# Kernel optimization log

Hardware: AMD Instinct MI355X
Metric: run time of the kernel (lower is better)

Reference implementation:

```python
import jax, jax.numpy as jnp
import numpy as np

D_MODEL = 1024
N_HEADS = 16
D_HEAD = D_MODEL // N_HEADS


def setup_inputs() -> dict:
    key = jax.random.key(0)
    ks = jax.random.split(key, 9)
    B, S = 2, 2048
    s = 0.02
    return {
        "x": jax.random.normal(ks[0], (B, S, D_MODEL), dtype=jnp.float32),
        "Wq": jax.random.normal(ks[1], (D_MODEL, D_MODEL), dtype=jnp.float32) * s,
        "bq": jnp.zeros((D_MODEL,), dtype=jnp.float32),
        "Wk": jax.random.normal(ks[2], (D_MODEL, D_MODEL), dtype=jnp.float32) * s,
        "bk": jnp.zeros((D_MODEL,), dtype=jnp.float32),
        "Wv": jax.random.normal(ks[3], (D_MODEL, D_MODEL), dtype=jnp.float32) * s,
        "bv": jnp.zeros((D_MODEL,), dtype=jnp.float32),
        "Wo": jax.random.normal(ks[4], (D_MODEL, D_MODEL), dtype=jnp.float32) * s,
        "bo": jnp.zeros((D_MODEL,), dtype=jnp.float32),
    }


def reference(x, Wq, bq, Wk, bk, Wv, bv, Wo, bo):
    B, S, _ = x.shape
    # projections -> [B, H, S, Dh]
    def split_heads(t):
        return t.reshape(B, S, N_HEADS, D_HEAD).transpose(0, 2, 1, 3)
    Q = split_heads(x @ Wq + bq)
    K = split_heads(x @ Wk + bk)
    V = split_heads(x @ Wv + bv)
    scores = jnp.einsum('bhqd,bhkd->bhqk', Q, K)  # [B,H,S,S]
    mask = jnp.tril(jnp.ones((S, S), dtype=bool))
    # NB: original masks BEFORE scaling (mask fill -1e9 then /sqrt(d_head))
    scores = jnp.where(mask[None, None], scores, jnp.float32(-1e9))
    scores = scores / jnp.sqrt(jnp.float32(D_HEAD))
    attn = jax.nn.softmax(scores, axis=-1)
    ctx = jnp.einsum('bhqk,bhkd->bhqd', attn, V)
    ctx = ctx.transpose(0, 2, 1, 3).reshape(B, S, D_MODEL)
    return ctx @ Wo + bo
```

## Files before the change

kernel.cpp:

```cpp
#include <hip/hip_runtime.h>

typedef __bf16 bf16;
typedef __bf16 bf16x8 __attribute__((ext_vector_type(8)));
typedef __bf16 bf16x4 __attribute__((ext_vector_type(4)));
typedef float  f32x4  __attribute__((ext_vector_type(4)));

#define D_MODEL 1024
#define S_LEN   2048
#define NHEAD   16
#define DHEAD   64
#define BATCH   2
#define MROWS   (BATCH * S_LEN)

#define QSCALE 0.18033688011112042f

__device__ __forceinline__ void gld_lds16(const void* g, void* lds_base) {
    __builtin_amdgcn_global_load_lds(
        (const __attribute__((address_space(1))) void*)g,
        (__attribute__((address_space(3))) void*)lds_base, 16, 0, 0);
}

__global__ void prep_kernel(const float* __restrict__ x,
                            const float* __restrict__ W0, const float* __restrict__ W1,
                            const float* __restrict__ W2, const float* __restrict__ W3,
                            bf16* __restrict__ xb, bf16* __restrict__ Wt) {
    int tx = threadIdx.x, ty = threadIdx.y;
    if (blockIdx.z == 4) {
        int tid = ty * 32 + tx;
        size_t base = ((size_t)blockIdx.y * 32 + blockIdx.x) * 4096;
#pragma unroll
        for (int j = 0; j < 4; j++) {
            size_t i = base + (size_t)(j * 256 + tid) * 4;
            f32x4 v = *(const f32x4*)(x + i);
            bf16x4 o;
            o[0] = (bf16)v[0]; o[1] = (bf16)v[1]; o[2] = (bf16)v[2]; o[3] = (bf16)v[3];
            *(bf16x4*)(xb + i) = o;
        }
        return;
    }
    __shared__ float tile[32][33];
    const float* W = (blockIdx.z == 0) ? W0 : (blockIdx.z == 1) ? W1
                   : (blockIdx.z == 2) ? W2 : W3;
    int n0 = blockIdx.x * 32, k0 = blockIdx.y * 32;
#pragma unroll
    for (int j = 0; j < 4; j++)
        tile[ty + 8 * j][tx] = W[(size_t)(k0 + ty + 8 * j) * D_MODEL + n0 + tx];
    __syncthreads();
    bf16* out = Wt + (size_t)blockIdx.z * D_MODEL * D_MODEL;
#pragma unroll
    for (int j = 0; j < 4; j++)
        out[(size_t)(n0 + ty + 8 * j) * D_MODEL + k0 + tx] = (bf16)tile[tx][ty + 8 * j];
}

template <int MODE>
__global__ __launch_bounds__(256, 2) void gemm_kernel(
    const bf16* __restrict__ A, const bf16* __restrict__ Bt,
    const float* __restrict__ b0, const float* __restrict__ b1, const float* __restrict__ b2,
    bf16* __restrict__ Qo, bf16* __restrict__ Ko, bf16* __restrict__ Vto,
    float* __restrict__ Co) {
    __shared__ bf16 sA[128 * 32];
    __shared__ bf16 sB[128 * 32];
    const int t = threadIdx.x;
    const int wave = t >> 6, lane = t & 63;
    const int wm = wave >> 1, wn = wave & 1;
    const int quad = lane >> 4, m16 = lane & 15;
    const int row0 = blockIdx.y * 128, col0 = blockIdx.x * 128;
    const int K = D_MODEL;

    f32x4 acc[4][4];
#pragma unroll
    for (int i = 0; i < 4; i++)
#pragma unroll
        for (int j = 0; j < 4; j++) acc[i][j] = (f32x4){0.f, 0.f, 0.f, 0.f};

    for (int kk = 0; kk < K; kk += 32) {
#pragma unroll
        for (int i = 0; i < 2; i++) {
            int cb = i * 256 + wave * 64;
            int c  = cb + lane;
            int r  = c >> 2, kg = c & 3;
            gld_lds16(A  + (size_t)(row0 + r) * K + kk + kg * 8, (char*)sA + cb * 16);
            gld_lds16(Bt + (size_t)(col0 + r) * K + kk + kg * 8, (char*)sB + cb * 16);
        }
        __syncthreads();
        bf16x8 af[4], bfr[4];
#pragma unroll
        for (int mi = 0; mi < 4; mi++)
            af[mi] = *(const bf16x8*)&sA[(wm * 64 + mi * 16 + m16) * 32 + quad * 8];
#pragma unroll
        for (int ni = 0; ni < 4; ni++)
            bfr[ni] = *(const bf16x8*)&sB[(wn * 64 + ni * 16 + m16) * 32 + quad * 8];
#pragma unroll
        for (int mi = 0; mi < 4; mi++)
#pragma unroll
            for (int ni = 0; ni < 4; ni++)
                acc[mi][ni] = __builtin_amdgcn_mfma_f32_16x16x32_bf16(
                    af[mi], bfr[ni], acc[mi][ni], 0, 0, 0);
        __syncthreads();
    }

    if (MODE == 1) {
#pragma unroll
        for (int mi = 0; mi < 4; mi++) {
            int r0 = row0 + wm * 64 + mi * 16 + quad * 4;
#pragma unroll
            for (int ni = 0; ni < 4; ni++) {
                int col = col0 + wn * 64 + ni * 16 + m16;
                float bias = b0[col];
#pragma unroll
                for (int r = 0; r < 4; r++)
                    Co[(size_t)(r0 + r) * D_MODEL + col] = acc[mi][ni][r] + bias;
            }
        }
    } else {
        int sel = col0 >> 10;
        const float* bias_arr = (sel == 0) ? b0 : (sel == 1) ? b1 : b2;
#pragma unroll
        for (int mi = 0; mi < 4; mi++) {
            int s0g = row0 + wm * 64 + mi * 16 + quad * 4;
            int b = s0g >> 11, ss0 = s0g & 2047;
#pragma unroll
            for (int ni = 0; ni < 4; ni++) {
                int col = col0 + wn * 64 + ni * 16 + m16;
                int cn = col & 1023;
                int h = cn >> 6, d = cn & 63;
                float bias = bias_arr[cn];
                if (sel < 2) {
                    bf16* dst = (sel == 0) ? Qo : Ko;
                    float scl = (sel == 0) ? QSCALE : 1.0f;
                    size_t base = (((size_t)b * NHEAD + h) * S_LEN);
#pragma unroll
                    for (int r = 0; r < 4; r++)
                        dst[(base + ss0 + r) * DHEAD + d] = (bf16)((acc[mi][ni][r] + bias) * scl);
                } else {
                    bf16x4 pk;
#pragma unroll
                    for (int r = 0; r < 4; r++) pk[r] = (bf16)(acc[mi][ni][r] + bias);
                    *(bf16x4*)(Vto + (((size_t)b * NHEAD + h) * DHEAD + d) * S_LEN + ss0) = pk;
                }
            }
        }
    }
}

__global__ __launch_bounds__(256, 3) void attn_kernel(
    const bf16* __restrict__ Q, const bf16* __restrict__ K,
    const bf16* __restrict__ Vt, bf16* __restrict__ ctx) {
    __shared__ bf16 Kt_s[2][64 * 64];
    __shared__ bf16 Vt_s[2][64 * 64];
    __shared__ bf16 P_s[4][2][16 * 72];

    const int t = threadIdx.x, wave = t >> 6, lane = t & 63;
    const int quad = lane >> 4, m16 = lane & 15;
    const int bh = blockIdx.y;
    const int tile = gridDim.x - 1 - blockIdx.x;
    const int q0 = tile * 128;
    const size_t qkbase = (size_t)bh * S_LEN * DHEAD;
    const int nt = 2 * tile + 2;

    bf16x8 aq[2][2];
#pragma unroll
    for (int g = 0; g < 2; g++)
#pragma unroll
        for (int kst = 0; kst < 2; kst++)
            aq[g][kst] = *(const bf16x8*)(Q + qkbase
                + (size_t)(q0 + wave * 32 + g * 16 + m16) * DHEAD + kst * 32 + quad * 8);

    f32x4 o[2][4];
#pragma unroll
    for (int g = 0; g < 2; g++)
#pragma unroll
        for (int di = 0; di < 4; di++) o[g][di] = (f32x4){0.f, 0.f, 0.f, 0.f};
    float l_acc[2] = {0.f, 0.f};

#pragma unroll
    for (int i = 0; i < 2; i++) {
        int cb = i * 256 + wave * 64;
        int c  = cb + lane;
        int pos = c >> 3, g = c & 7;
        int gk = g ^ (pos & 7);
        gld_lds16(K  + qkbase + (size_t)pos * DHEAD + gk * 8, (char*)&Kt_s[0][0] + cb * 16);
        gld_lds16(Vt + qkbase + (size_t)pos * S_LEN + gk * 8, (char*)&Vt_s[0][0] + cb * 16);
    }
    __syncthreads();

    for (int it = 0; it < nt; ++it) {
        const int cur = it & 1;
        const int kt0 = it * 64;
        if (it + 1 < nt) {
            const int ktn = kt0 + 64;
#pragma unroll
            for (int i = 0; i < 2; i++) {
                int cb = i * 256 + wave * 64;
                int c  = cb + lane;
                int pos = c >> 3, g = c & 7;
                int gk = g ^ (pos & 7);
                gld_lds16(K  + qkbase + (size_t)(ktn + pos) * DHEAD + gk * 8,
                          (char*)&Kt_s[cur ^ 1][0] + cb * 16);
                gld_lds16(Vt + qkbase + (size_t)pos * S_LEN + ktn + gk * 8,
                          (char*)&Vt_s[cur ^ 1][0] + cb * 16);
            }
        }

        f32x4 sc[2][4];
#pragma unroll
        for (int g = 0; g < 2; g++)
#pragma unroll
            for (int ni = 0; ni < 4; ni++) sc[g][ni] = (f32x4){0.f, 0.f, 0.f, 0.f};
#pragma unroll
        for (int ni = 0; ni < 4; ni++) {
            int pos = ni * 16 + m16;
#pragma unroll
            for (int kst = 0; kst < 2; kst++) {
                int gg = (kst * 4 + quad) ^ (pos & 7);
                bf16x8 kf = *(const bf16x8*)&Kt_s[cur][pos * 64 + gg * 8];
#pragma unroll
                for (int g = 0; g < 2; g++)
                    sc[g][ni] = __builtin_amdgcn_mfma_f32_16x16x32_bf16(
                        kf, aq[g][kst], sc[g][ni], 0, 0, 0);
            }
        }
#pragma unroll
        for (int g = 0; g < 2; g++) {
            int rowbase = q0 + wave * 32 + g * 16;
            if (kt0 + 63 > rowbase) {
                int qg = rowbase + m16;
#pragma unroll
                for (int ni = 0; ni < 4; ni++)
#pragma unroll
                    for (int r = 0; r < 4; r++) {
                        int kp = kt0 + ni * 16 + quad * 4 + r;
                        if (kp > qg) sc[g][ni][r] = -1e9f;
                    }
            }
        }
#pragma unroll
        for (int g = 0; g < 2; g++) {
            bf16* Pw = &P_s[wave][g][0];
            float ls = 0.f;
#pragma unroll
            for (int ni = 0; ni < 4; ni++) {
                bf16x4 pk;
#pragma unroll
                for (int r = 0; r < 4; r++) {
                    float p = __builtin_amdgcn_exp2f(sc[g][ni][r]);
                    ls += p;
                    pk[r] = (bf16)p;
                }
                *(bf16x4*)&Pw[m16 * 72 + ni * 16 + quad * 4] = pk;
            }
            l_acc[g] += ls;
        }

#pragma unroll
        for (int kst = 0; kst < 2; kst++) {
            bf16x8 ap[2];
#pragma unroll
            for (int g = 0; g < 2; g++)
                ap[g] = *(const bf16x8*)&P_s[wave][g][m16 * 72 + kst * 32 + quad * 8];
#pragma unroll
            for (int di = 0; di < 4; di++) {
                int d = di * 16 + m16;
                int gg = (kst * 4 + quad) ^ (d & 7);
                bf16x8 vf = *(const bf16x8*)&Vt_s[cur][d * 64 + gg * 8];
#pragma unroll
                for (int g = 0; g < 2; g++)
                    o[g][di] = __builtin_amdgcn_mfma_f32_16x16x32_bf16(
                        vf, ap[g], o[g][di], 0, 0, 0);
            }
        }
        __syncthreads();
    }

    int b = bh >> 4, h = bh & 15;
#pragma unroll
    for (int g = 0; g < 2; g++) {
        float l = l_acc[g];
        l += __shfl_xor(l, 16);
        l += __shfl_xor(l, 32);
        float rl = 1.0f / l;
        int s = q0 + wave * 32 + g * 16 + m16;
#pragma unroll
        for (int di = 0; di < 4; di++) {
            bf16x4 pk;
#pragma unroll
            for (int r = 0; r < 4; r++) pk[r] = (bf16)(o[g][di][r] * rl);
            *(bf16x4*)(ctx + ((size_t)b * S_LEN + s) * D_MODEL
                       + h * DHEAD + di * 16 + quad * 4) = pk;
        }
    }
}

extern "C" void kernel_launch(void* const* d_in, const int* in_sizes, int n_in,
                              void* d_out, int out_size, void* d_ws, size_t ws_size,
                              hipStream_t stream) {
    const float* x  = (const float*)d_in[0];
    const float* Wq = (const float*)d_in[1];
    const float* bq = (const float*)d_in[2];
    const float* Wk = (const float*)d_in[3];
    const float* bk = (const float*)d_in[4];
    const float* Wv = (const float*)d_in[5];
    const float* bv = (const float*)d_in[6];
    const float* Wo = (const float*)d_in[7];
    const float* bo = (const float*)d_in[8];
    float* out = (float*)d_out;

    char* ws = (char*)d_ws;
    const size_t MB = 1u << 20;
    bf16* xb  = (bf16*)(ws + 0);
    bf16* Wt  = (bf16*)(ws + 8  * MB);
    bf16* Qb  = (bf16*)(ws + 16 * MB);
    bf16* Kb  = (bf16*)(ws + 24 * MB);
    bf16* Vtb = (bf16*)(ws + 32 * MB);
    bf16* ctx = (bf16*)(ws + 0);

    prep_kernel<<<dim3(32, 32, 5), dim3(32, 8), 0, stream>>>(x, Wq, Wk, Wv, Wo, xb, Wt);
    gemm_kernel<0><<<dim3(24, 32), 256, 0, stream>>>(xb, Wt, bq, bk, bv,
                                                     Qb, Kb, Vtb, nullptr);
    attn_kernel<<<dim3(16, 32), 256, 0, stream>>>(Qb, Kb, Vtb, ctx);
    gemm_kernel<1><<<dim3(8, 32), 256, 0, stream>>>(ctx, Wt + 3 * 1024 * 1024,
                                                    bo, nullptr, nullptr,
                                                    nullptr, nullptr, nullptr, out);
}
```

Before: 201.1 us.

## Pair causal query tiles for balanced work and triple-buffer K/V loads

Each block now processes two 64-row query tiles, p and 31-p, so every block does the same amount of causal work instead of a variable amount per 128-row tile. K/V staging moves to a three-deep LDS ring with one barrier per step, using explicit vmcnt waits in place of the end-of-loop __syncthreads. The mask is applied only on each tile's diagonal block. In exchange LDS use grows, the launch bound drops to 2 blocks per CU, and the inline-asm waitcnt depends on the load count per stage.

Measured after the change: 191.0 us. 1.05x faster.

```diff
diff --git a/kernel.cpp b/kernel.cpp
--- a/kernel.cpp
+++ b/kernel.cpp
@@ -143,148 +143,151 @@
     }
 }
 
-__global__ __launch_bounds__(256, 3) void attn_kernel(
+__global__ __launch_bounds__(256, 2) void attn_kernel(
     const bf16* __restrict__ Q, const bf16* __restrict__ K,
     const bf16* __restrict__ Vt, bf16* __restrict__ ctx) {
-    __shared__ bf16 Kt_s[2][64 * 64];
-    __shared__ bf16 Vt_s[2][64 * 64];
+    __shared__ bf16 Kt_s[3][64 * 64];
+    __shared__ bf16 Vt_s[3][64 * 64];
     __shared__ bf16 P_s[4][2][16 * 72];
 
     const int t = threadIdx.x, wave = t >> 6, lane = t & 63;
     const int quad = lane >> 4, m16 = lane & 15;
-    const int bh = blockIdx.y;
-    const int tile = gridDim.x - 1 - blockIdx.x;
-    const int q0 = tile * 128;
-    const size_t qkbase = (size_t)bh * S_LEN * DHEAD;
-    const int nt = 2 * tile + 2;
+    const int bh = blockIdx.y, p = blockIdx.x;
+    const int tT[2] = {p, 31 - p};
+    const int nt = 32 - p;
+    const size_t base = (size_t)bh * S_LEN * DHEAD;
 
     bf16x8 aq[2][2];
 #pragma unroll
-    for (int g = 0; g < 2; g++)
+    for (int it = 0; it < 2; it++)
 #pragma unroll
         for (int kst = 0; kst < 2; kst++)
-            aq[g][kst] = *(const bf16x8*)(Q + qkbase
-                + (size_t)(q0 + wave * 32 + g * 16 + m16) * DHEAD + kst * 32 + quad * 8);
+            aq[it][kst] = *(const bf16x8*)(Q + base
+                + (size_t)(tT[it] * 64 + wave * 16 + m16) * DHEAD + kst * 32 + quad * 8);
 
     f32x4 o[2][4];
 #pragma unroll
-    for (int g = 0; g < 2; g++)
-#pragma unroll
-        for (int di = 0; di < 4; di++) o[g][di] = (f32x4){0.f, 0.f, 0.f, 0.f};
+    for (int it = 0; it < 2; it++)
+#pragma unroll
+        for (int di = 0; di < 4; di++) o[it][di] = (f32x4){0.f, 0.f, 0.f, 0.f};
     float l_acc[2] = {0.f, 0.f};
 
-#pragma unroll
-    for (int i = 0; i < 2; i++) {
-        int cb = i * 256 + wave * 64;
-        int c  = cb + lane;
-        int pos = c >> 3, g = c & 7;
-        int gk = g ^ (pos & 7);
-        gld_lds16(K  + qkbase + (size_t)pos * DHEAD + gk * 8, (char*)&Kt_s[0][0] + cb * 16);
-        gld_lds16(Vt + qkbase + (size_t)pos * S_LEN + gk * 8, (char*)&Vt_s[0][0] + cb * 16);
-    }
-    __syncthreads();
-
-    for (int it = 0; it < nt; ++it) {
-        const int cur = it & 1;
-        const int kt0 = it * 64;
-        if (it + 1 < nt) {
-            const int ktn = kt0 + 64;
-#pragma unroll
-            for (int i = 0; i < 2; i++) {
-                int cb = i * 256 + wave * 64;
-                int c  = cb + lane;
-                int pos = c >> 3, g = c & 7;
-                int gk = g ^ (pos & 7);
-                gld_lds16(K  + qkbase + (size_t)(ktn + pos) * DHEAD + gk * 8,
-                          (char*)&Kt_s[cur ^ 1][0] + cb * 16);
-                gld_lds16(Vt + qkbase + (size_t)pos * S_LEN + ktn + gk * 8,
-                          (char*)&Vt_s[cur ^ 1][0] + cb * 16);
-            }
-        }
-
-        f32x4 sc[2][4];
-#pragma unroll
-        for (int g = 0; g < 2; g++)
-#pragma unroll
-            for (int ni = 0; ni < 4; ni++) sc[g][ni] = (f32x4){0.f, 0.f, 0.f, 0.f};
-#pragma unroll
-        for (int ni = 0; ni < 4; ni++) {
-            int pos = ni * 16 + m16;
+    auto stage = [&](int j, int buf) {
+#pragma unroll
+        for (int i = 0; i < 2; i++) {
+            int cb = i * 256 + wave * 64;
+            int c  = cb + lane;
+            int pos = c >> 3, g = c & 7;
+            int gk = g ^ (pos & 7);
+            gld_lds16(K  + base + (size_t)(j * 64 + pos) * DHEAD + gk * 8,
+                      (char*)&Kt_s[buf][0] + cb * 16);
+            gld_lds16(Vt + base + (size_t)pos * S_LEN + j * 64 + gk * 8,
+                      (char*)&Vt_s[buf][0] + cb * 16);
+        }
+    };
+
+    stage(0, 0);
+    if (nt > 1) stage(1, 1);
+
+    for (int j = 0; j < nt; ++j) {
+        if (j + 1 < nt) asm volatile("s_waitcnt vmcnt(4)\n\ts_barrier" ::: "memory");
+        else            asm volatile("s_waitcnt vmcnt(0)\n\ts_barrier" ::: "memory");
+        if (j + 2 < nt) stage(j + 2, (j + 2) % 3);
+
+        const int cur = j % 3;
+        const bool aAct = (j <= tT[0]);
+        const int kt0 = j * 64;
+
+        auto computeTile = [&](bool both) {
+            int itlo = both ? 0 : 1;
+            f32x4 sc[2][4];
+#pragma unroll
+            for (int it = 0; it < 2; it++)
+#pragma unroll
+                for (int ni = 0; ni < 4; ni++) sc[it][ni] = (f32x4){0.f, 0.f, 0.f, 0.f};
+#pragma unroll
+            for (int ni = 0; ni < 4; ni++) {
+                int pos = ni * 16 + m16;
+#pragma unroll
+                for (int kst = 0; kst < 2; kst++) {
+                    int gg = (kst * 4 + quad) ^ (pos & 7);
+                    bf16x8 kf = *(const bf16x8*)&Kt_s[cur][pos * 64 + gg * 8];
+                    sc[1][ni] = __builtin_amdgcn_mfma_f32_16x16x32_bf16(
+                        kf, aq[1][kst], sc[1][ni], 0, 0, 0);
+                    if (both)
+                        sc[0][ni] = __builtin_amdgcn_mfma_f32_16x16x32_bf16(
+                            kf, aq[0][kst], sc[0][ni], 0, 0, 0);
+                }
+            }
+#pragma unroll
+            for (int it = 0; it < 2; it++) {
+                if (it < itlo) continue;
+                if (j == tT[it]) {
+                    int qg = tT[it] * 64 + wave * 16 + m16;
+#pragma unroll
+                    for (int ni = 0; ni < 4; ni++)
+#pragma unroll
+                        for (int r = 0; r < 4; r++) {
+                            int kp = kt0 + ni * 16 + quad * 4 + r;
+                            if (kp > qg) sc[it][ni][r] = -1e9f;
+                        }
+                }
+            }
+#pragma unroll
+            for (int it = 0; it < 2; it++) {
+                if (it < itlo) continue;
+                bf16* Pw = &P_s[wave][it][0];
+                float ls = 0.f;
+#pragma unroll
+                for (int ni = 0; ni < 4; ni++) {
+                    bf16x4 pk;
+#pragma unroll
+                    for (int r = 0; r < 4; r++) {
+                        float pe = __builtin_amdgcn_exp2f(sc[it][ni][r]);
+                        ls += pe;
+                        pk[r] = (bf16)pe;
+                    }
+                    *(bf16x4*)&Pw[m16 * 72 + ni * 16 + quad * 4] = pk;
+                }
+                l_acc[it] += ls;
+            }
 #pragma unroll
             for (int kst = 0; kst < 2; kst++) {
-                int gg = (kst * 4 + quad) ^ (pos & 7);
-                bf16x8 kf = *(const bf16x8*)&Kt_s[cur][pos * 64 + gg * 8];
-#pragma unroll
-                for (int g = 0; g < 2; g++)
-                    sc[g][ni] = __builtin_amdgcn_mfma_f32_16x16x32_bf16(
-                        kf, aq[g][kst], sc[g][ni], 0, 0, 0);
-            }
-        }
-#pragma unroll
-        for (int g = 0; g < 2; g++) {
-            int rowbase = q0 + wave * 32 + g * 16;
-            if (kt0 + 63 > rowbase) {
-                int qg = rowbase + m16;
-#pragma unroll
-                for (int ni = 0; ni < 4; ni++)
-#pragma unroll
-                    for (int r = 0; r < 4; r++) {
-                        int kp = kt0 + ni * 16 + quad * 4 + r;
-                        if (kp > qg) sc[g][ni][r] = -1e9f;
-                    }
-            }
-        }
-#pragma unroll
-        for (int g = 0; g < 2; g++) {
-            bf16* Pw = &P_s[wave][g][0];
-            float ls = 0.f;
-#pragma unroll
-            for (int ni = 0; ni < 4; ni++) {
-                bf16x4 pk;
-#pragma unroll
-                for (int r = 0; r < 4; r++) {
-                    float p = __builtin_amdgcn_exp2f(sc[g][ni][r]);
-                    ls += p;
-                    pk[r] = (bf16)p;
-                }
-                *(bf16x4*)&Pw[m16 * 72 + ni * 16 + quad * 4] = pk;
-            }
-            l_acc[g] += ls;
-        }
-
-#pragma unroll
-        for (int kst = 0; kst < 2; kst++) {
-            bf16x8 ap[2];
-#pragma unroll
-            for (int g = 0; g < 2; g++)
-                ap[g] = *(const bf16x8*)&P_s[wave][g][m16 * 72 + kst * 32 + quad * 8];
-#pragma unroll
-            for (int di = 0; di < 4; di++) {
-                int d = di * 16 + m16;
-                int gg = (kst * 4 + quad) ^ (d & 7);
-                bf16x8 vf = *(const bf16x8*)&Vt_s[cur][d * 64 + gg * 8];
-#pragma unroll
-                for (int g = 0; g < 2; g++)
-                    o[g][di] = __builtin_amdgcn_mfma_f32_16x16x32_bf16(
-                        vf, ap[g], o[g][di], 0, 0, 0);
-            }
-        }
-        __syncthreads();
+                bf16x8 ap[2];
+#pragma unroll
+                for (int it = 0; it < 2; it++)
+                    if (it >= itlo)
+                        ap[it] = *(const bf16x8*)&P_s[wave][it][m16 * 72 + kst * 32 + quad * 8];
+#pragma unroll
+                for (int di = 0; di < 4; di++) {
+                    int d = di * 16 + m16;
+                    int gg = (kst * 4 + quad) ^ (d & 7);
+                    bf16x8 vf = *(const bf16x8*)&Vt_s[cur][d * 64 + gg * 8];
+                    o[1][di] = __builtin_amdgcn_mfma_f32_16x16x32_bf16(
+                        vf, ap[1], o[1][di], 0, 0, 0);
+                    if (both)
+                        o[0][di] = __builtin_amdgcn_mfma_f32_16x16x32_bf16(
+                            vf, ap[0], o[0][di], 0, 0, 0);
+                }
+            }
+        };
+        if (aAct) computeTile(true);
+        else      computeTile(false);
     }
 
     int b = bh >> 4, h = bh & 15;
 #pragma unroll
-    for (int g = 0; g < 2; g++) {
-        float l = l_acc[g];
+    for (int it = 0; it < 2; it++) {
+        float l = l_acc[it];
         l += __shfl_xor(l, 16);
         l += __shfl_xor(l, 32);
         float rl = 1.0f / l;
-        int s = q0 + wave * 32 + g * 16 + m16;
+        int s = tT[it] * 64 + wave * 16 + m16;
 #pragma unroll
         for (int di = 0; di < 4; di++) {
             bf16x4 pk;
 #pragma unroll
-            for (int r = 0; r < 4; r++) pk[r] = (bf16)(o[g][di][r] * rl);
+            for (int r = 0; r < 4; r++) pk[r] = (bf16)(o[it][di][r] * rl);
             *(bf16x4*)(ctx + ((size_t)b * S_LEN + s) * D_MODEL
                        + h * DHEAD + di * 16 + quad * 4) = pk;
         }
```
